# Kernel tuning notes

Measured on AMD Instinct MI355X. Metric: run time of the kernel, lower is better.

## Reference

```python
import jax, jax.numpy as jnp
import numpy as np
from jax import lax

B, T, H, W, C = 2, 16, 64, 64, 64
KT, K = 3, 3


def kernel_to_freq_3d(kernel, T, H, W):
    # kernel: (C, k_t, k_h, k_w) -> (C, T, H, W) complex freq response
    Cc, k_t, k_h, k_w = kernel.shape
    t_idx = (jnp.arange(k_t) - k_t // 2) % T
    h_idx = (jnp.arange(k_h) - k_h // 2) % H
    w_idx = (jnp.arange(k_w) - k_w // 2) % W
    tt, th, tw = jnp.meshgrid(t_idx, h_idx, w_idx, indexing='ij')
    padded = jnp.zeros((Cc, T, H, W), dtype=kernel.dtype).at[:, tt, th, tw].set(kernel)
    return jnp.fft.fftn(padded, axes=(1, 2, 3))


def mamba_op(left, right):
    a1, b1 = left
    a2, b2 = right
    return (a1 * a2, a2 * b1 + b2)


def setup_inputs() -> dict:
    key = jax.random.key(0)
    ks = jax.random.split(key, 8)
    fan_in = KT * K * K
    x = jax.random.normal(ks[0], (B, T, H, W, C), dtype=jnp.float32)
    A_kernel = jax.random.normal(ks[1], (C, KT, K, K), dtype=jnp.float32) / np.sqrt(fan_in)
    B_kernel = jax.random.normal(ks[2], (C, KT, K, K), dtype=jnp.float32) / np.sqrt(fan_in)
    forget_bias = jnp.full((C,), 2.0, dtype=jnp.float32)
    forget_scale = jnp.full((C,), 0.01, dtype=jnp.float32)
    input_bias = jnp.zeros((C,), dtype=jnp.float32)
    input_scale = jnp.full((C,), 0.01, dtype=jnp.float32)
    delta_W = jax.random.normal(ks[3], (C, C), dtype=jnp.float32) / np.sqrt(C)
    delta_b = jnp.zeros((C,), dtype=jnp.float32)
    return {"x": x, "A_kernel": A_kernel, "B_kernel": B_kernel,
            "forget_bias": forget_bias, "forget_scale": forget_scale,
            "input_bias": input_bias, "input_scale": input_scale,
            "delta_W": delta_W, "delta_b": delta_b}


def reference(x, A_kernel, B_kernel, forget_bias, forget_scale,
              input_bias, input_scale, delta_W, delta_b):
    Bb, Tt, Hh, Ww, Cc = x.shape
    # freq-domain kernels: (C,T,H,W) -> (T,1,H,W,C) for broadcasting over batch
    A_f = kernel_to_freq_3d(A_kernel, Tt, Hh, Ww).transpose(1, 2, 3, 0)[:, None]
    B_f = kernel_to_freq_3d(B_kernel, Tt, Hh, Ww).transpose(1, 2, 3, 0)[:, None]
    # input-dependent gates (real, elementwise per channel)
    forget_gate = jax.nn.sigmoid(forget_bias + forget_scale * x)
    input_gate = jax.nn.sigmoid(input_bias + input_scale * x)
    delta = jax.nn.softplus(jnp.einsum('bthwc,cd->bthwd', x, delta_W) + delta_b)
    x_f = jnp.fft.fftn(x, axes=(1, 2, 3))  # complex (B,T,H,W,C)
    # move time axis to front for the scan: (T,B,H,W,C)
    a_seq = forget_gate.transpose(1, 0, 2, 3, 4) * A_f
    b_seq = (input_gate.transpose(1, 0, 2, 3, 4)
             * delta.transpose(1, 0, 2, 3, 4)
             * B_f * x_f.transpose(1, 0, 2, 3, 4))
    _, h_all_f = lax.associative_scan(mamba_op, (a_seq, b_seq), axis=0)
    h_f = h_all_f.transpose(1, 0, 2, 3, 4)
    h = jnp.fft.ifftn(h_f, axes=(1, 2, 3)).real
    return h.astype(x.dtype)
```

## Files before the change

### kernel.cpp

```cpp
#include <hip/hip_runtime.h>
#include <math.h>

#define Bb 2
#define Tt 16
#define Hh 64
#define Ww 64
#define Cc 64
#define ST_ (Hh*Ww*Cc)
#define SH_ (Ww*Cc)
#define SB_ (Tt*Hh*Ww*Cc)
#define XELEMS (Bb*Tt*Hh*Ww*Cc)

#define TWO_PI 6.2831853071795864769f

typedef __attribute__((ext_vector_type(8))) short bf16x8;
typedef __attribute__((ext_vector_type(4))) float f32x4;

__device__ __forceinline__ float2 cmul(float2 a, float2 b) {
    return make_float2(fmaf(a.x, b.x, -a.y * b.y), fmaf(a.x, b.y, a.y * b.x));
}
__device__ __forceinline__ float2 cadd(float2 a, float2 b) { return make_float2(a.x + b.x, a.y + b.y); }
__device__ __forceinline__ float2 csub(float2 a, float2 b) { return make_float2(a.x - b.x, a.y - b.y); }

__device__ __forceinline__ unsigned bfpack(float2 f) {
    unsigned r = __float_as_uint(f.x);
    unsigned i = __float_as_uint(f.y);
    r = (r + 0x7fffu + ((r >> 16) & 1u)) >> 16;
    i = (i + 0x7fffu + ((i >> 16) & 1u)) >> 16;
    return r | (i << 16);
}
__device__ __forceinline__ float2 bfunpack(unsigned u) {
    return make_float2(__uint_as_float(u << 16), __uint_as_float(u & 0xffff0000u));
}

template <int S>
__device__ __forceinline__ void fft8(float2 v[8]) {
    const float R = 0.70710678118654752f;
    float2 s0 = cadd(v[0], v[4]), d0 = csub(v[0], v[4]);
    float2 s1 = cadd(v[1], v[5]), d1 = csub(v[1], v[5]);
    float2 s2 = cadd(v[2], v[6]), d2 = csub(v[2], v[6]);
    float2 s3 = cadd(v[3], v[7]), d3 = csub(v[3], v[7]);
    d1 = make_float2(R * (d1.x - (float)S * d1.y), R * ((float)S * d1.x + d1.y));
    { float2 t = d2; d2 = make_float2(-(float)S * t.y, (float)S * t.x); }
    d3 = make_float2(R * (-d3.x - (float)S * d3.y), R * ((float)S * d3.x - d3.y));
    float2 u0 = cadd(s0, s2), u2 = csub(s0, s2);
    float2 u1 = cadd(s1, s3), u3t = csub(s1, s3);
    float2 u3 = make_float2(-(float)S * u3t.y, (float)S * u3t.x);
    v[0] = cadd(u0, u1); v[1] = csub(u0, u1); v[2] = cadd(u2, u3); v[3] = csub(u2, u3);
    float2 w0 = cadd(d0, d2), w2 = csub(d0, d2);
    float2 w1 = cadd(d1, d3), w3t = csub(d1, d3);
    float2 w3 = make_float2(-(float)S * w3t.y, (float)S * w3t.x);
    v[4] = cadd(w0, w1); v[5] = csub(w0, w1); v[6] = cadd(w2, w3); v[7] = csub(w2, w3);
}

template <int S>
__device__ __forceinline__ void fft4(float2& a, float2& b, float2& c, float2& d) {
    float2 t0 = cadd(a, c), t1 = csub(a, c);
    float2 t2 = cadd(b, d), t3 = csub(b, d);
    a = cadd(t0, t2);
    c = csub(t0, t2);
    b = make_float2(t1.x - (float)S * t3.y, t1.y + (float)S * t3.x);
    d = make_float2(t1.x + (float)S * t3.y, t1.y - (float)S * t3.x);
}

template <int S>
__device__ __forceinline__ void fft16(float2 v[16]) {
    const float CS[10] = {1.f, 0.92387953f, 0.70710678f, 0.38268343f, 0.f,
                          -0.38268343f, -0.70710678f, -0.92387953f, -1.f, -0.92387953f};
    const float SN[10] = {0.f, 0.38268343f, 0.70710678f, 0.92387953f, 1.f,
                          0.92387953f, 0.70710678f, 0.38268343f, 0.f, -0.38268343f};
    float2 A[4][4];
#pragma unroll
    for (int j = 0; j < 4; ++j) {
        A[j][0] = v[j]; A[j][1] = v[4 + j]; A[j][2] = v[8 + j]; A[j][3] = v[12 + j];
        fft4<S>(A[j][0], A[j][1], A[j][2], A[j][3]);
#pragma unroll
        for (int k0 = 0; k0 < 4; ++k0) {
            int m = j * k0;
            float2 tw = make_float2(CS[m], (float)S * SN[m]);
            A[j][k0] = cmul(A[j][k0], tw);
        }
    }
#pragma unroll
    for (int k0 = 0; k0 < 4; ++k0) {
        fft4<S>(A[0][k0], A[1][k0], A[2][k0], A[3][k0]);
        v[k0] = A[0][k0]; v[k0 + 4] = A[1][k0]; v[k0 + 8] = A[2][k0]; v[k0 + 12] = A[3][k0];
    }
}

__global__ __launch_bounds__(256, 4) void k_fft_w_fwd(const float* __restrict__ x,
                                                      unsigned* __restrict__ X,
                                                      const float* __restrict__ dW,
                                                      unsigned* __restrict__ pre) {
    __shared__ unsigned ex[64 * 65];
    const int brev[8] = {0, 4, 2, 6, 1, 5, 3, 7};
    int tid = threadIdx.x;

    if (blockIdx.x == 0) {
        for (int i = tid; i < 2048; i += 256) {
            int p2 = i & 3, lane = (i >> 2) & 63, ka = (i >> 8) & 1, nt = i >> 9;
            int kb = ka * 32 + (lane >> 4) * 8 + 2 * p2;
            int ccol = (lane & 15) + 16 * nt;
            pre[i] = bfpack(make_float2(dW[kb * 64 + ccol], dW[(kb + 1) * 64 + ccol]));
        }
    }

    int j = tid >> 5, cl = tid & 31;
    int base = blockIdx.x * 4096;
    float2 v[2][8];
#pragma unroll
    for (int q = 0; q < 2; ++q) {
        int c = cl + 32 * q;
#pragma unroll
        for (int n1 = 0; n1 < 8; ++n1)
            v[q][n1] = make_float2(x[base + (8 * n1 + j) * 64 + c], 0.f);
    }
    float sj, cj; sincosf(-TWO_PI * (float)j / 64.f, &sj, &cj);
    float2 w1 = make_float2(cj, sj);
#pragma unroll
    for (int q = 0; q < 2; ++q) {
        fft8<-1>(v[q]);
        int c = cl + 32 * q;
        float2 tw = make_float2(1.f, 0.f);
#pragma unroll
        for (int k0 = 0; k0 < 8; ++k0) {
            ex[c * 65 + j * 8 + k0] = bfpack(cmul(v[q][brev[k0]], tw));
            tw = cmul(tw, w1);
        }
    }
    __syncthreads();
#pragma unroll
    for (int q = 0; q < 2; ++q) {
        int c = cl + 32 * q;
        float2 z[8];
#pragma unroll
        for (int n0 = 0; n0 < 8; ++n0) z[n0] = bfunpack(ex[c * 65 + n0 * 8 + j]);
        fft8<-1>(z);
#pragma unroll
        for (int m = 0; m < 8; ++m)
            X[base + (j + 8 * brev[m]) * 64 + c] = bfpack(z[m]);
    }
}

template <int S, int SHIFT>
__global__ __launch_bounds__(256, 4) void k_fft_h(unsigned* __restrict__ X) {
    __shared__ unsigned ex[64 * 65];
    const int brev[8] = {0, 4, 2, 6, 1, 5, 3, 7};
    const float sc = 1.0f / (float)(1 << SHIFT);
    int tid = threadIdx.x;
    int j = tid >> 5, cl = tid & 31;
    int s = blockIdx.x;
    int bt = s >> 6, w = s & 63;
    int base = bt * ST_ + w * 64;
    float2 v[2][8];
#pragma unroll
    for (int q = 0; q < 2; ++q) {
        int c = cl + 32 * q;
#pragma unroll
        for (int n1 = 0; n1 < 8; ++n1)
            v[q][n1] = bfunpack(X[base + (8 * n1 + j) * SH_ + c]);
    }
    float sj, cj; sincosf((float)S * TWO_PI * (float)j / 64.f, &sj, &cj);
    float2 w1 = make_float2(cj, sj);
#pragma unroll
    for (int q = 0; q < 2; ++q) {
        fft8<S>(v[q]);
        int c = cl + 32 * q;
        float2 tw = make_float2(1.f, 0.f);
#pragma unroll
        for (int k0 = 0; k0 < 8; ++k0) {
            ex[c * 65 + j * 8 + k0] = bfpack(cmul(v[q][brev[k0]], tw));
            tw = cmul(tw, w1);
        }
    }
    __syncthreads();
#pragma unroll
    for (int q = 0; q < 2; ++q) {
        int c = cl + 32 * q;
        float2 z[8];
#pragma unroll
        for (int n0 = 0; n0 < 8; ++n0) z[n0] = bfunpack(ex[c * 65 + n0 * 8 + j]);
        fft8<S>(z);
#pragma unroll
        for (int m = 0; m < 8; ++m) {
            float2 o = make_float2(z[m].x * sc, z[m].y * sc);
            X[base + (j + 8 * brev[m]) * SH_ + c] = bfpack(o);
        }
    }
}

__global__ __launch_bounds__(256) void k_mid(
    const float* __restrict__ x, unsigned* __restrict__ X,
    const float* __restrict__ Ak, const float* __restrict__ Bk,
    const float* __restrict__ fb, const float* __restrict__ fs,
    const float* __restrict__ ib, const float* __restrict__ isc_,
    const uint4* __restrict__ pre, const float* __restrict__ db) {
    const float CT[16] = {1.f, 0.9238795f, 0.7071068f, 0.3826834f, 0.f, -0.3826834f,
                          -0.7071068f, -0.9238795f, -1.f, -0.9238795f, -0.7071068f,
                          -0.3826834f, 0.f, 0.3826834f, 0.7071068f, 0.9238795f};
    const float SN[16] = {0.f, 0.3826834f, 0.7071068f, 0.9238795f, 1.f, 0.9238795f,
                          0.7071068f, 0.3826834f, 0.f, -0.3826834f, -0.7071068f,
                          -0.9238795f, -1.f, -0.9238795f, -0.7071068f, -0.3826834f};
    __shared__ float Akl[1728], Bkl[1728];
    __shared__ __align__(16) float xs[4][16 * 68 + 4];

    int tid = threadIdx.x;
    int g = tid >> 6, lane = tid & 63;
    int c = lane;
    int site = blockIdx.x * 4 + g;
    int b = site >> 12, hw = site & 4095;
    int h = hw >> 6, w = hw & 63;
    int base = b * SB_ + hw * 64;

    for (int i = tid; i < 1728; i += 256) { Akl[i] = Ak[i]; Bkl[i] = Bk[i]; }

    float xv[16];
    float2 v[16];
#pragma unroll
    for (int t = 0; t < 16; ++t) {
        xv[t] = x[base + t * ST_ + c];
        v[t] = bfunpack(X[base + t * ST_ + c]);
    }
#pragma unroll
    for (int t = 0; t < 16; ++t) xs[g][t * 68 + c] = xv[t];
    __syncthreads();

    int m = lane & 15, q = lane >> 4;
    bf16x8 Afrag[2];
#pragma unroll
    for (int ka = 0; ka < 2; ++ka) {
        int d0 = ka * 32 + q * 8;
        const float* p = &xs[g][m * 68 + d0];
        float4 f0 = *(const float4*)p;
        float4 f1 = *(const float4*)(p + 4);
        union { bf16x8 v8; unsigned u[4]; } U;
        U.u[0] = bfpack(make_float2(f0.x, f0.y));
        U.u[1] = bfpack(make_float2(f0.z, f0.w));
        U.u[2] = bfpack(make_float2(f1.x, f1.y));
        U.u[3] = bfpack(make_float2(f1.z, f1.w));
        Afrag[ka] = U.v8;
    }
#pragma unroll
    for (int nt = 0; nt < 4; ++nt) {
        int ccol = m + 16 * nt;
        float dbn = db[ccol];
        f32x4 acc = {dbn, dbn, dbn, dbn};
#pragma unroll
        for (int ka = 0; ka < 2; ++ka) {
            union { bf16x8 v8; uint4 u4; } Ub;
            Ub.u4 = pre[(nt * 2 + ka) * 64 + lane];
            acc = __builtin_amdgcn_mfma_f32_16x16x32_bf16(Afrag[ka], Ub.v8, acc, 0, 0, 0);
        }
#pragma unroll
        for (int reg = 0; reg < 4; ++reg)
            xs[g][(q * 4 + reg) * 68 + ccol] = acc[reg];
    }

    float sh, ch; sincosf(TWO_PI * (float)h / 64.0f, &sh, &ch);
    float sw, cw; sincosf(TWO_PI * (float)w / 64.0f, &sw, &cw);
    float2 eh[3] = { make_float2(ch, sh), make_float2(1.f, 0.f), make_float2(ch, -sh) };
    float2 ew[3] = { make_float2(cw, sw), make_float2(1.f, 0.f), make_float2(cw, -sw) };
    float2 GA[3], GB[3];
#pragma unroll
    for (int kt = 0; kt < 3; ++kt) { GA[kt] = make_float2(0.f, 0.f); GB[kt] = make_float2(0.f, 0.f); }
#pragma unroll
    for (int kh = 0; kh < 3; ++kh) {
#pragma unroll
        for (int kw = 0; kw < 3; ++kw) {
            float2 e = cmul(eh[kh], ew[kw]);
#pragma unroll
            for (int kt = 0; kt < 3; ++kt) {
                float ka = Akl[c * 27 + kt * 9 + kh * 3 + kw];
                float kb = Bkl[c * 27 + kt * 9 + kh * 3 + kw];
                GA[kt].x = fmaf(ka, e.x, GA[kt].x);
                GA[kt].y = fmaf(ka, e.y, GA[kt].y);
                GB[kt].x = fmaf(kb, e.x, GB[kt].x);
                GB[kt].y = fmaf(kb, e.y, GB[kt].y);
            }
        }
    }
    float fbc = fb[c], fsc = fs[c], ibc = ib[c], iscv = isc_[c];

    fft16<-1>(v);
    __syncthreads();

    float delta_raw[16];
#pragma unroll
    for (int t = 0; t < 16; ++t) delta_raw[t] = xs[g][t * 68 + c];

    float2 hv = make_float2(0.f, 0.f);
#pragma unroll
    for (int t = 0; t < 16; ++t) {
        float ct = CT[t], st = SN[t];
        float2 Af, Bf;
        Af.x = GA[1].x + ct * (GA[0].x + GA[2].x) - st * (GA[0].y - GA[2].y);
        Af.y = GA[1].y + ct * (GA[0].y + GA[2].y) + st * (GA[0].x - GA[2].x);
        Bf.x = GB[1].x + ct * (GB[0].x + GB[2].x) - st * (GB[0].y - GB[2].y);
        Bf.y = GB[1].y + ct * (GB[0].y + GB[2].y) + st * (GB[0].x - GB[2].x);

        float xc = xv[t];
        float fg  = __builtin_amdgcn_rcpf(1.f + __expf(-(fbc + fsc * xc)));
        float igv = __builtin_amdgcn_rcpf(1.f + __expf(-(ibc + iscv * xc)));
        float dot = delta_raw[t];
        float delta = (dot > 20.f) ? dot : __logf(1.f + __expf(dot));

        float sR = igv * delta;
        float2 bbv;
        bbv.x = sR * (Bf.x * v[t].x - Bf.y * v[t].y);
        bbv.y = sR * (Bf.x * v[t].y + Bf.y * v[t].x);
        float2 av = make_float2(fg * Af.x, fg * Af.y);
        float2 nh;
        nh.x = av.x * hv.x - av.y * hv.y + bbv.x;
        nh.y = av.x * hv.y + av.y * hv.x + bbv.y;
        hv = nh;
        v[t] = hv;
    }

    fft16<1>(v);

#pragma unroll
    for (int t = 0; t < 16; ++t) {
        float2 o = make_float2(v[t].x * 0.0625f, v[t].y * 0.0625f);
        X[base + t * ST_ + c] = bfpack(o);
    }
}

__global__ __launch_bounds__(256, 4) void k_fft_w_inv_out(const unsigned* __restrict__ X,
                                                          float* __restrict__ out) {
    __shared__ unsigned ex[64 * 65];
    const int brev[8] = {0, 4, 2, 6, 1, 5, 3, 7};
    int tid = threadIdx.x;
    int j = tid >> 5, cl = tid & 31;
    int base = blockIdx.x * 4096;
    float2 v[2][8];
#pragma unroll
    for (int q = 0; q < 2; ++q) {
        int c = cl + 32 * q;
#pragma unroll
        for (int n1 = 0; n1 < 8; ++n1)
            v[q][n1] = bfunpack(X[base + (8 * n1 + j) * 64 + c]);
    }
    float sj, cj; sincosf(TWO_PI * (float)j / 64.f, &sj, &cj);
    float2 w1 = make_float2(cj, sj);
#pragma unroll
    for (int q = 0; q < 2; ++q) {
        fft8<1>(v[q]);
        int c = cl + 32 * q;
        float2 tw = make_float2(1.f, 0.f);
#pragma unroll
        for (int k0 = 0; k0 < 8; ++k0) {
            ex[c * 65 + j * 8 + k0] = bfpack(cmul(v[q][brev[k0]], tw));
            tw = cmul(tw, w1);
        }
    }
    __syncthreads();
#pragma unroll
    for (int q = 0; q < 2; ++q) {
        int c = cl + 32 * q;
        float2 z[8];
#pragma unroll
        for (int n0 = 0; n0 < 8; ++n0) z[n0] = bfunpack(ex[c * 65 + n0 * 8 + j]);
        fft8<1>(z);
#pragma unroll
        for (int m = 0; m < 8; ++m)
            out[base + (j + 8 * brev[m]) * 64 + c] = z[m].x * (1.0f / 64.0f);
    }
}

extern "C" void kernel_launch(void* const* d_in, const int* in_sizes, int n_in,
                              void* d_out, int out_size, void* d_ws, size_t ws_size,
                              hipStream_t stream) {
    const float* x   = (const float*)d_in[0];
    const float* Ak  = (const float*)d_in[1];
    const float* Bk  = (const float*)d_in[2];
    const float* fb  = (const float*)d_in[3];
    const float* fs  = (const float*)d_in[4];
    const float* ib  = (const float*)d_in[5];
    const float* is_ = (const float*)d_in[6];
    const float* dW  = (const float*)d_in[7];
    const float* db  = (const float*)d_in[8];
    float* out = (float*)d_out;
    unsigned* X = (unsigned*)d_ws;
    unsigned* pre = (unsigned*)((char*)d_ws + (size_t)XELEMS * 4);

    k_fft_w_fwd<<<Bb * Tt * Hh, 256, 0, stream>>>(x, X, dW, pre);
    k_fft_h<-1, 0><<<Bb * Tt * Ww, 256, 0, stream>>>(X);
    k_mid<<<(Bb * Hh * Ww) / 4, 256, 0, stream>>>(x, X, Ak, Bk, fb, fs, ib, is_,
                                                  (const uint4*)pre, db);
    k_fft_h<1, 6><<<Bb * Tt * Ww, 256, 0, stream>>>(X);
    k_fft_w_inv_out<<<Bb * Tt * Hh, 256, 0, stream>>>(X, out);
}
```

Measured before the change: 173.6 us.

## Replace radix-8 FFTs along W and H with bf16 MFMA dense DFT matmuls

Swaps the shared-memory radix-8x8 FFT kernels for the W and H axes for dense 64-point DFTs computed as bf16 MFMA matrix multiplies. The DFT matrices are built in bf16 by a new setup kernel and stored in the workspace. Inverse scaling is folded into those tables, and the real-output inverse-W pass keeps only the real row. The aim is to move butterfly arithmetic and shuffle traffic onto matrix cores, at the cost of more total FLOPs, an extra launch, and extra bf16 rounding in the twiddle matrices.

Measured after the change: 186.1 us. 7.2% more time.

```diff
diff --git a/kernel.cpp b/kernel.cpp
--- a/kernel.cpp
+++ b/kernel.cpp
@@ -16,6 +16,12 @@
 typedef __attribute__((ext_vector_type(8))) short bf16x8;
 typedef __attribute__((ext_vector_type(4))) float f32x4;
 
+#define OFF_PRE  8388608u
+#define OFF_TWF  8390656u
+#define OFF_THF  8394752u
+#define OFF_THI  8402944u
+#define OFF_TWI  8411136u
+
 __device__ __forceinline__ float2 cmul(float2 a, float2 b) {
     return make_float2(fmaf(a.x, b.x, -a.y * b.y), fmaf(a.x, b.y, a.y * b.x));
 }
@@ -31,26 +37,6 @@
 }
 __device__ __forceinline__ float2 bfunpack(unsigned u) {
     return make_float2(__uint_as_float(u << 16), __uint_as_float(u & 0xffff0000u));
-}
-
-template <int S>
-__device__ __forceinline__ void fft8(float2 v[8]) {
-    const float R = 0.70710678118654752f;
-    float2 s0 = cadd(v[0], v[4]), d0 = csub(v[0], v[4]);
-    float2 s1 = cadd(v[1], v[5]), d1 = csub(v[1], v[5]);
-    float2 s2 = cadd(v[2], v[6]), d2 = csub(v[2], v[6]);
-    float2 s3 = cadd(v[3], v[7]), d3 = csub(v[3], v[7]);
-    d1 = make_float2(R * (d1.x - (float)S * d1.y), R * ((float)S * d1.x + d1.y));
-    { float2 t = d2; d2 = make_float2(-(float)S * t.y, (float)S * t.x); }
-    d3 = make_float2(R * (-d3.x - (float)S * d3.y), R * ((float)S * d3.x - d3.y));
-    float2 u0 = cadd(s0, s2), u2 = csub(s0, s2);
-    float2 u1 = cadd(s1, s3), u3t = csub(s1, s3);
-    float2 u3 = make_float2(-(float)S * u3t.y, (float)S * u3t.x);
-    v[0] = cadd(u0, u1); v[1] = csub(u0, u1); v[2] = cadd(u2, u3); v[3] = csub(u2, u3);
-    float2 w0 = cadd(d0, d2), w2 = csub(d0, d2);
-    float2 w1 = cadd(d1, d3), w3t = csub(d1, d3);
-    float2 w3 = make_float2(-(float)S * w3t.y, (float)S * w3t.x);
-    v[4] = cadd(w0, w1); v[5] = csub(w0, w1); v[6] = cadd(w2, w3); v[7] = csub(w2, w3);
 }
 
 template <int S>
@@ -88,103 +74,195 @@
     }
 }
 
-__global__ __launch_bounds__(256, 4) void k_fft_w_fwd(const float* __restrict__ x,
-                                                      unsigned* __restrict__ X,
-                                                      const float* __restrict__ dW,
-                                                      unsigned* __restrict__ pre) {
-    __shared__ unsigned ex[64 * 65];
-    const int brev[8] = {0, 4, 2, 6, 1, 5, 3, 7};
+__global__ __launch_bounds__(256) void k_setup(const float* __restrict__ dW,
+                                               unsigned* __restrict__ ws) {
+    int j = blockIdx.x * 256 + threadIdx.x;
+    if (j < 2048) {
+        int p2 = j & 3, lane = (j >> 2) & 63, ka = (j >> 8) & 1, nt = j >> 9;
+        int kb = ka * 32 + (lane >> 4) * 8 + 2 * p2;
+        int ccol = (lane & 15) + 16 * nt;
+        ws[OFF_PRE + j] = bfpack(make_float2(dW[kb * 64 + ccol], dW[(kb + 1) * 64 + ccol]));
+        return;
+    }
+    int idx, table;
+    if (j < 6144)       { idx = j - 2048;  table = 0; }
+    else if (j < 14336) { idx = j - 6144;  table = 1; }
+    else if (j < 22528) { idx = j - 14336; table = 2; }
+    else                { idx = j - 22528; table = 3; }
+    int p = idx & 3;
+    int lane = (idx >> 2) & 63;
+    int m = lane & 15, q = lane >> 4;
+    int ka, r, reim;
+    if (table == 0)      { ka = (idx >> 8) & 1; r = (idx >> 9) & 3;  reim = (idx >> 11) & 1; }
+    else if (table == 3) { ka = (idx >> 8) & 3; r = (idx >> 10) & 3; reim = 0; }
+    else                 { ka = (idx >> 8) & 3; r = (idx >> 10) & 3; reim = (idx >> 12) & 1; }
+    int wp = r * 16 + m;
+    int k0 = ka * 32 + q * 8 + 2 * p;
+    float val[2];
+#pragma unroll
+    for (int dk = 0; dk < 2; ++dk) {
+        int k = k0 + dk;
+        float v;
+        if (table == 0) {
+            int a = (wp * k) & 63;
+            float sn, cs; sincosf(TWO_PI * (float)a * (1.0f / 64.0f), &sn, &cs);
+            v = (reim == 0) ? cs : -sn;
+        } else {
+            int h = k >> 1;
+            int a = (wp * h) & 63;
+            float sn, cs; sincosf(TWO_PI * (float)a * (1.0f / 64.0f), &sn, &cs);
+            bool even = (k & 1) == 0;
+            if (table == 1) {
+                v = (reim == 0) ? (even ? cs : sn) : (even ? -sn : cs);
+            } else if (table == 2) {
+                v = (reim == 0) ? (even ? cs : -sn) : (even ? sn : cs);
+                v *= (1.0f / 64.0f);
+            } else {
+                v = (even ? cs : -sn) * (1.0f / 64.0f);
+            }
+        }
+        val[dk] = v;
+    }
+    unsigned base = (table == 0) ? OFF_TWF : (table == 1) ? OFF_THF
+                  : (table == 2) ? OFF_THI : OFF_TWI;
+    ws[base + idx] = bfpack(make_float2(val[0], val[1]));
+}
+
+__global__ __launch_bounds__(256) void k_dft_w_fwd(const float* __restrict__ x,
+                                                   unsigned* __restrict__ X,
+                                                   const uint4* __restrict__ T) {
+    __shared__ float xsl[64 * 65];
     int tid = threadIdx.x;
-
-    if (blockIdx.x == 0) {
-        for (int i = tid; i < 2048; i += 256) {
-            int p2 = i & 3, lane = (i >> 2) & 63, ka = (i >> 8) & 1, nt = i >> 9;
-            int kb = ka * 32 + (lane >> 4) * 8 + 2 * p2;
-            int ccol = (lane & 15) + 16 * nt;
-            pre[i] = bfpack(make_float2(dW[kb * 64 + ccol], dW[(kb + 1) * 64 + ccol]));
-        }
-    }
-
-    int j = tid >> 5, cl = tid & 31;
-    int base = blockIdx.x * 4096;
-    float2 v[2][8];
-#pragma unroll
-    for (int q = 0; q < 2; ++q) {
-        int c = cl + 32 * q;
-#pragma unroll
-        for (int n1 = 0; n1 < 8; ++n1)
-            v[q][n1] = make_float2(x[base + (8 * n1 + j) * 64 + c], 0.f);
-    }
-    float sj, cj; sincosf(-TWO_PI * (float)j / 64.f, &sj, &cj);
-    float2 w1 = make_float2(cj, sj);
-#pragma unroll
-    for (int q = 0; q < 2; ++q) {
-        fft8<-1>(v[q]);
-        int c = cl + 32 * q;
-        float2 tw = make_float2(1.f, 0.f);
-#pragma unroll
-        for (int k0 = 0; k0 < 8; ++k0) {
-            ex[c * 65 + j * 8 + k0] = bfpack(cmul(v[q][brev[k0]], tw));
-            tw = cmul(tw, w1);
-        }
-    }
+    int sbase = blockIdx.x * 4096;
+    for (int i = tid; i < 4096; i += 256)
+        xsl[(i >> 6) * 65 + (i & 63)] = x[sbase + i];
     __syncthreads();
-#pragma unroll
-    for (int q = 0; q < 2; ++q) {
-        int c = cl + 32 * q;
-        float2 z[8];
-#pragma unroll
-        for (int n0 = 0; n0 < 8; ++n0) z[n0] = bfunpack(ex[c * 65 + n0 * 8 + j]);
-        fft8<-1>(z);
-#pragma unroll
-        for (int m = 0; m < 8; ++m)
-            X[base + (j + 8 * brev[m]) * 64 + c] = bfpack(z[m]);
-    }
-}
-
-template <int S, int SHIFT>
-__global__ __launch_bounds__(256, 4) void k_fft_h(unsigned* __restrict__ X) {
-    __shared__ unsigned ex[64 * 65];
-    const int brev[8] = {0, 4, 2, 6, 1, 5, 3, 7};
-    const float sc = 1.0f / (float)(1 << SHIFT);
+
+    int r = tid >> 6, lane = tid & 63;
+    int m = lane & 15, q = lane >> 4;
+    union U48 { uint4 u4; unsigned u[4]; bf16x8 v8; };
+    U48 Are[2], Aim[2], Bf;
+#pragma unroll
+    for (int ka = 0; ka < 2; ++ka) {
+        Are[ka].u4 = T[((0 * 4 + r) * 2 + ka) * 64 + lane];
+        Aim[ka].u4 = T[((1 * 4 + r) * 2 + ka) * 64 + lane];
+    }
+    f32x4 ar[4], ai[4];
+#pragma unroll
+    for (int nt = 0; nt < 4; ++nt) { ar[nt] = (f32x4){0.f,0.f,0.f,0.f}; ai[nt] = (f32x4){0.f,0.f,0.f,0.f}; }
+#pragma unroll
+    for (int nt = 0; nt < 4; ++nt) {
+        int cc = m + 16 * nt;
+#pragma unroll
+        for (int ka = 0; ka < 2; ++ka) {
+            int w0 = ka * 32 + q * 8;
+#pragma unroll
+            for (int p = 0; p < 4; ++p)
+                Bf.u[p] = bfpack(make_float2(xsl[(w0 + 2 * p) * 65 + cc],
+                                             xsl[(w0 + 2 * p + 1) * 65 + cc]));
+            ar[nt] = __builtin_amdgcn_mfma_f32_16x16x32_bf16(Are[ka].v8, Bf.v8, ar[nt], 0, 0, 0);
+            ai[nt] = __builtin_amdgcn_mfma_f32_16x16x32_bf16(Aim[ka].v8, Bf.v8, ai[nt], 0, 0, 0);
+        }
+    }
+#pragma unroll
+    for (int nt = 0; nt < 4; ++nt) {
+        int cc = m + 16 * nt;
+#pragma unroll
+        for (int reg = 0; reg < 4; ++reg) {
+            int wp = r * 16 + q * 4 + reg;
+            X[sbase + wp * 64 + cc] = bfpack(make_float2(ar[nt][reg], ai[nt][reg]));
+        }
+    }
+}
+
+__global__ __launch_bounds__(256) void k_dft_h(unsigned* __restrict__ X,
+                                               const uint4* __restrict__ T) {
+    __shared__ unsigned zs[64 * 68];
     int tid = threadIdx.x;
-    int j = tid >> 5, cl = tid & 31;
     int s = blockIdx.x;
     int bt = s >> 6, w = s & 63;
     int base = bt * ST_ + w * 64;
-    float2 v[2][8];
-#pragma unroll
-    for (int q = 0; q < 2; ++q) {
-        int c = cl + 32 * q;
-#pragma unroll
-        for (int n1 = 0; n1 < 8; ++n1)
-            v[q][n1] = bfunpack(X[base + (8 * n1 + j) * SH_ + c]);
-    }
-    float sj, cj; sincosf((float)S * TWO_PI * (float)j / 64.f, &sj, &cj);
-    float2 w1 = make_float2(cj, sj);
-#pragma unroll
-    for (int q = 0; q < 2; ++q) {
-        fft8<S>(v[q]);
-        int c = cl + 32 * q;
-        float2 tw = make_float2(1.f, 0.f);
-#pragma unroll
-        for (int k0 = 0; k0 < 8; ++k0) {
-            ex[c * 65 + j * 8 + k0] = bfpack(cmul(v[q][brev[k0]], tw));
-            tw = cmul(tw, w1);
-        }
-    }
+    for (int i = tid; i < 4096; i += 256)
+        zs[(i >> 6) * 68 + (i & 63)] = X[base + (i >> 6) * SH_ + (i & 63)];
     __syncthreads();
-#pragma unroll
-    for (int q = 0; q < 2; ++q) {
-        int c = cl + 32 * q;
-        float2 z[8];
-#pragma unroll
-        for (int n0 = 0; n0 < 8; ++n0) z[n0] = bfunpack(ex[c * 65 + n0 * 8 + j]);
-        fft8<S>(z);
-#pragma unroll
-        for (int m = 0; m < 8; ++m) {
-            float2 o = make_float2(z[m].x * sc, z[m].y * sc);
-            X[base + (j + 8 * brev[m]) * SH_ + c] = bfpack(o);
+
+    int r = tid >> 6, lane = tid & 63;
+    int m = lane & 15, q = lane >> 4;
+    union U48 { uint4 u4; unsigned u[4]; bf16x8 v8; };
+    U48 Are[4], Aim[4], Bf;
+#pragma unroll
+    for (int ka = 0; ka < 4; ++ka) {
+        Are[ka].u4 = T[((0 * 4 + r) * 4 + ka) * 64 + lane];
+        Aim[ka].u4 = T[((1 * 4 + r) * 4 + ka) * 64 + lane];
+    }
+    f32x4 ar[4], ai[4];
+#pragma unroll
+    for (int nt = 0; nt < 4; ++nt) { ar[nt] = (f32x4){0.f,0.f,0.f,0.f}; ai[nt] = (f32x4){0.f,0.f,0.f,0.f}; }
+#pragma unroll
+    for (int nt = 0; nt < 4; ++nt) {
+        int cc = m + 16 * nt;
+#pragma unroll
+        for (int ka = 0; ka < 4; ++ka) {
+            int h0 = ka * 16 + q * 4;
+            Bf.u[0] = zs[(h0 + 0) * 68 + cc];
+            Bf.u[1] = zs[(h0 + 1) * 68 + cc];
+            Bf.u[2] = zs[(h0 + 2) * 68 + cc];
+            Bf.u[3] = zs[(h0 + 3) * 68 + cc];
+            ar[nt] = __builtin_amdgcn_mfma_f32_16x16x32_bf16(Are[ka].v8, Bf.v8, ar[nt], 0, 0, 0);
+            ai[nt] = __builtin_amdgcn_mfma_f32_16x16x32_bf16(Aim[ka].v8, Bf.v8, ai[nt], 0, 0, 0);
+        }
+    }
+#pragma unroll
+    for (int nt = 0; nt < 4; ++nt) {
+        int cc = m + 16 * nt;
+#pragma unroll
+        for (int reg = 0; reg < 4; ++reg) {
+            int hp = r * 16 + q * 4 + reg;
+            X[base + hp * SH_ + cc] = bfpack(make_float2(ar[nt][reg], ai[nt][reg]));
+        }
+    }
+}
+
+__global__ __launch_bounds__(256) void k_dft_w_inv(const unsigned* __restrict__ X,
+                                                   float* __restrict__ out,
+                                                   const uint4* __restrict__ T) {
+    __shared__ unsigned zs[64 * 68];
+    int tid = threadIdx.x;
+    int sbase = blockIdx.x * 4096;
+    for (int i = tid; i < 4096; i += 256)
+        zs[(i >> 6) * 68 + (i & 63)] = X[sbase + i];
+    __syncthreads();
+
+    int r = tid >> 6, lane = tid & 63;
+    int m = lane & 15, q = lane >> 4;
+    union U48 { uint4 u4; unsigned u[4]; bf16x8 v8; };
+    U48 Are[4], Bf;
+#pragma unroll
+    for (int ka = 0; ka < 4; ++ka)
+        Are[ka].u4 = T[(r * 4 + ka) * 64 + lane];
+    f32x4 ar[4];
+#pragma unroll
+    for (int nt = 0; nt < 4; ++nt) ar[nt] = (f32x4){0.f,0.f,0.f,0.f};
+#pragma unroll
+    for (int nt = 0; nt < 4; ++nt) {
+        int cc = m + 16 * nt;
+#pragma unroll
+        for (int ka = 0; ka < 4; ++ka) {
+            int w0 = ka * 16 + q * 4;
+            Bf.u[0] = zs[(w0 + 0) * 68 + cc];
+            Bf.u[1] = zs[(w0 + 1) * 68 + cc];
+            Bf.u[2] = zs[(w0 + 2) * 68 + cc];
+            Bf.u[3] = zs[(w0 + 3) * 68 + cc];
+            ar[nt] = __builtin_amdgcn_mfma_f32_16x16x32_bf16(Are[ka].v8, Bf.v8, ar[nt], 0, 0, 0);
+        }
+    }
+#pragma unroll
+    for (int nt = 0; nt < 4; ++nt) {
+        int cc = m + 16 * nt;
+#pragma unroll
+        for (int reg = 0; reg < 4; ++reg) {
+            int wp = r * 16 + q * 4 + reg;
+            out[sbase + wp * 64 + cc] = ar[nt][reg];
         }
     }
 }
@@ -325,48 +403,6 @@
     }
 }
 
-__global__ __launch_bounds__(256, 4) void k_fft_w_inv_out(const unsigned* __restrict__ X,
-                                                          float* __restrict__ out) {
-    __shared__ unsigned ex[64 * 65];
-    const int brev[8] = {0, 4, 2, 6, 1, 5, 3, 7};
-    int tid = threadIdx.x;
-    int j = tid >> 5, cl = tid & 31;
-    int base = blockIdx.x * 4096;
-    float2 v[2][8];
-#pragma unroll
-    for (int q = 0; q < 2; ++q) {
-        int c = cl + 32 * q;
-#pragma unroll
-        for (int n1 = 0; n1 < 8; ++n1)
-            v[q][n1] = bfunpack(X[base + (8 * n1 + j) * 64 + c]);
-    }
-    float sj, cj; sincosf(TWO_PI * (float)j / 64.f, &sj, &cj);
-    float2 w1 = make_float2(cj, sj);
-#pragma unroll
-    for (int q = 0; q < 2; ++q) {
-        fft8<1>(v[q]);
-        int c = cl + 32 * q;
-        float2 tw = make_float2(1.f, 0.f);
-#pragma unroll
-        for (int k0 = 0; k0 < 8; ++k0) {
-            ex[c * 65 + j * 8 + k0] = bfpack(cmul(v[q][brev[k0]], tw));
-            tw = cmul(tw, w1);
-        }
-    }
-    __syncthreads();
-#pragma unroll
-    for (int q = 0; q < 2; ++q) {
-        int c = cl + 32 * q;
-        float2 z[8];
-#pragma unroll
-        for (int n0 = 0; n0 < 8; ++n0) z[n0] = bfunpack(ex[c * 65 + n0 * 8 + j]);
-        fft8<1>(z);
-#pragma unroll
-        for (int m = 0; m < 8; ++m)
-            out[base + (j + 8 * brev[m]) * 64 + c] = z[m].x * (1.0f / 64.0f);
-    }
-}
-
 extern "C" void kernel_launch(void* const* d_in, const int* in_sizes, int n_in,
                               void* d_out, int out_size, void* d_ws, size_t ws_size,
                               hipStream_t stream) {
@@ -380,13 +416,14 @@
     const float* dW  = (const float*)d_in[7];
     const float* db  = (const float*)d_in[8];
     float* out = (float*)d_out;
-    unsigned* X = (unsigned*)d_ws;
-    unsigned* pre = (unsigned*)((char*)d_ws + (size_t)XELEMS * 4);
-
-    k_fft_w_fwd<<<Bb * Tt * Hh, 256, 0, stream>>>(x, X, dW, pre);
-    k_fft_h<-1, 0><<<Bb * Tt * Ww, 256, 0, stream>>>(X);
+    unsigned* ws = (unsigned*)d_ws;
+    unsigned* X = ws;
+
+    k_setup<<<104, 256, 0, stream>>>(dW, ws);
+    k_dft_w_fwd<<<Bb * Tt * Hh, 256, 0, stream>>>(x, X, (const uint4*)(ws + OFF_TWF));
+    k_dft_h<<<Bb * Tt * Ww, 256, 0, stream>>>(X, (const uint4*)(ws + OFF_THF));
     k_mid<<<(Bb * Hh * Ww) / 4, 256, 0, stream>>>(x, X, Ak, Bk, fb, fs, ib, is_,
-                                                  (const uint4*)pre, db);
-    k_fft_h<1, 6><<<Bb * Tt * Ww, 256, 0, stream>>>(X);
-    k_fft_w_inv_out<<<Bb * Tt * Hh, 256, 0, stream>>>(X, out);
-}
+                                                  (const uint4*)(ws + OFF_PRE), db);
+    k_dft_h<<<Bb * Tt * Ww, 256, 0, stream>>>(X, (const uint4*)(ws + OFF_THI));
+    k_dft_w_inv<<<Bb * Tt * Hh, 256, 0, stream>>>(X, out, (const uint4*)(ws + OFF_TWI));
+}
```
